# Optimization experiments

Measured on AMD Instinct MI355X. Metric: run time of the kernel, lower is better.

Reference implementation:

```python
import math
import jax, jax.numpy as jnp
import numpy as np

DIM = 1024
QK_DIM = 200
HIDDEN = 2 * DIM  # expansion_factor = 2
N = 8192


def setup_inputs() -> dict:
    key = jax.random.key(0)
    ks = jax.random.split(key, 8)
    s = 0.02
    return {
        "x": jax.random.normal(ks[0], (N, DIM), dtype=jnp.float32),
        "W_hidden": jax.random.normal(ks[1], (DIM, 2 * HIDDEN), dtype=jnp.float32) * s,
        "b_hidden": jnp.zeros((2 * HIDDEN,), dtype=jnp.float32),
        "W_qk": jax.random.normal(ks[2], (DIM, QK_DIM), dtype=jnp.float32) * s,
        "b_qk": jnp.zeros((QK_DIM,), dtype=jnp.float32),
        "gamma": 1.0 + jax.random.normal(ks[3], (2, QK_DIM), dtype=jnp.float32) * s,
        "beta": jnp.zeros((2, QK_DIM), dtype=jnp.float32),
        "W_out": jax.random.normal(ks[4], (HIDDEN, DIM), dtype=jnp.float32) * s,
        "b_out": jnp.zeros((DIM,), dtype=jnp.float32),
    }


def reference(x, W_hidden, b_hidden, W_qk, b_qk, gamma, beta, W_out, b_out):
    # to_hidden: Linear(dim -> 2*hidden) + SiLU, then chunk into v, gate
    hid = jax.nn.silu(x @ W_hidden + b_hidden)        # [N, 2H]
    v, gate = jnp.split(hid, 2, axis=-1)              # [N, H] each
    # to_qk: Linear(dim -> qk_dim) + SiLU
    qk = jax.nn.silu(x @ W_qk + b_qk)                 # [N, qk]
    # OffsetScale (heads=2): per-head affine on the shared qk
    q = qk * gamma[0] + beta[0]                       # [N, qk]
    k = qk * gamma[1] + beta[1]                       # [N, qk]
    # scores scaled by sqrt(dim) (module uses self.dim, not qk_dim)
    sim = (q @ k.T) * (1.0 / math.sqrt(x.shape[-1]))  # [N, N]
    # ReLU-squared attention (no softmax); dropout=0.0 -> identity
    attn = jnp.square(jax.nn.relu(sim))
    out = attn @ v                                    # [N, H]
    out = out * gate
    out = out @ W_out + b_out                         # [N, dim]
    # add_residual=True in this module multiplies by x
    return out * x
```

## Files before the change

kernel.cpp:

```cpp
#include <hip/hip_runtime.h>
#include <stdint.h>


typedef __bf16 bf16x8 __attribute__((ext_vector_type(8)));
typedef float f32x4 __attribute__((ext_vector_type(4)));

__device__ __forceinline__ uint16_t f2bf(float f) {
  uint32_t u = __builtin_bit_cast(uint32_t, f);
  u += 0x7fffu + ((u >> 16) & 1u);
  return (uint16_t)(u >> 16);
}
__device__ __forceinline__ float silu_f(float s) {
  return s / (1.f + __expf(-s));
}

__device__ __forceinline__ void gload16(const void* g, void* l) {
  __builtin_amdgcn_global_load_lds(
      (__attribute__((address_space(1))) void*)const_cast<void*>(g),
      (__attribute__((address_space(3))) void*)l, 16, 0, 0);
}


__global__ void cast_to_bf16(const float* __restrict__ in, uint16_t* __restrict__ out, int n4) {
  int i = blockIdx.x * blockDim.x + threadIdx.x;
  if (i < n4) {
    float4 f = ((const float4*)in)[i];
    ushort4 o;
    o.x = f2bf(f.x); o.y = f2bf(f.y); o.z = f2bf(f.z); o.w = f2bf(f.w);
    ((ushort4*)out)[i] = o;
  }
}

__global__ void transpose_cast_pad(const float* __restrict__ in, uint16_t* __restrict__ out,
                                   int R, int C, int Cp) {
  __shared__ float tile[32][33];
  int cb = blockIdx.x * 32;
  int rb = blockIdx.y * 32;
  int tx = threadIdx.x;
  int ty = threadIdx.y;
#pragma unroll
  for (int i = 0; i < 4; ++i) {
    int r = rb + ty + i * 8;
    int c = cb + tx;
    tile[ty + i * 8][tx] = (c < C) ? in[(size_t)r * C + c] : 0.f;
  }
  __syncthreads();
#pragma unroll
  for (int i = 0; i < 4; ++i) {
    int c = cb + ty + i * 8;
    if (c < Cp) out[(size_t)c * R + rb + tx] = f2bf(tile[tx][ty + i * 8]);
  }
}


struct EpiParams {
  const float* bias;
  const float* bias2;
  const float* g0;
  const float* b0;
  const float* g1;
  const float* b1;
  const uint16_t* gate;
  const float* x;
  uint16_t* o16a;
  uint16_t* o16b;
  uint16_t* oq;
  uint16_t* ok;
  float* o32;
};

__global__ __launch_bounds__(256) void k_hidqk(
    const uint16_t* __restrict__ A, const uint16_t* __restrict__ Bt, EpiParams p) {
  __shared__ __align__(16) uint16_t SH[128 * 64];
  uint16_t* As = SH;
  uint16_t* Bs = SH + 4096;

  const int tid = threadIdx.x;
  const int lane = tid & 63;
  const int wave = tid >> 6;
  const int wr = (wave >> 1) * 64;
  const int wc = (wave & 1) * 64;
  const int m0 = blockIdx.y * 128;
  const int n0 = blockIdx.x * 128;
  const int lda = 1024, ldb = 1024, K = 1024;

  f32x4 acc[4][4] = {};

  const int r0 = tid >> 2;
  const int q8 = (tid & 3) * 8;
  const uint16_t* gA0 = A + (size_t)(m0 + r0) * lda + q8;
  const uint16_t* gA1 = A + (size_t)(m0 + 64 + r0) * lda + q8;
  const uint16_t* gB0 = Bt + (size_t)(n0 + r0) * ldb + q8;
  const uint16_t* gB1 = Bt + (size_t)(n0 + 64 + r0) * ldb + q8;
  uint16_t* lA0 = As + wave * 512;
  uint16_t* lA1 = As + 2048 + wave * 512;
  uint16_t* lB0 = Bs + wave * 512;
  uint16_t* lB1 = Bs + 2048 + wave * 512;

  const int fr = lane & 15;
  const int rg = lane >> 4;
  const int kq = rg * 8;

  for (int k0 = 0; k0 < K; k0 += 32) {
    __syncthreads();
    gload16(gA0 + k0, lA0);
    gload16(gA1 + k0, lA1);
    gload16(gB0 + k0, lB0);
    gload16(gB1 + k0, lB1);
    __syncthreads();

    bf16x8 a[4], b[4];
#pragma unroll
    for (int i = 0; i < 4; ++i)
      a[i] = *(const bf16x8*)(As + (wr + i * 16 + fr) * 32 + kq);
#pragma unroll
    for (int j = 0; j < 4; ++j)
      b[j] = *(const bf16x8*)(Bs + (wc + j * 16 + fr) * 32 + kq);
#pragma unroll
    for (int i = 0; i < 4; ++i)
#pragma unroll
      for (int j = 0; j < 4; ++j)
        acc[i][j] = __builtin_amdgcn_mfma_f32_16x16x32_bf16(a[i], b[j], acc[i][j], 0, 0, 0);
  }

  if (n0 < 2048) {
    __syncthreads();
    uint16_t* ar = SH + wave * 2048;
    const int lrow = lane >> 3;
    const int mc = (lane & 7) * 8;
#pragma unroll
    for (int j = 0; j < 4; ++j) {
      const float bc = p.bias[n0 + wc + j * 16 + fr];
#pragma unroll
      for (int i = 0; i < 4; ++i)
#pragma unroll
        for (int r = 0; r < 4; ++r)
          ar[fr * 72 + i * 16 + rg * 4 + r] = f2bf(silu_f(acc[i][j][r] + bc));
#pragma unroll
      for (int rr = 0; rr < 2; ++rr) {
        bf16x8 v = *(const bf16x8*)(ar + (rr * 8 + lrow) * 72 + mc);
        *(bf16x8*)(p.o16a + (size_t)(n0 + wc + j * 16 + rr * 8 + lrow) * 8192 + m0 + wr + mc) = v;
      }
    }
  } else if (n0 < 4096) {
    __syncthreads();
    uint16_t* ar = SH + wave * 2048;
    const int lrow = lane >> 3;
    const int nc = (lane & 7) * 8;
    float bc[4];
#pragma unroll
    for (int j = 0; j < 4; ++j) bc[j] = p.bias[n0 + wc + j * 16 + fr];
#pragma unroll
    for (int i = 0; i < 4; ++i) {
#pragma unroll
      for (int j = 0; j < 4; ++j)
#pragma unroll
        for (int r = 0; r < 4; ++r)
          ar[(rg * 4 + r) * 72 + j * 16 + fr] = f2bf(silu_f(acc[i][j][r] + bc[j]));
#pragma unroll
      for (int rr = 0; rr < 2; ++rr) {
        bf16x8 v = *(const bf16x8*)(ar + (rr * 8 + lrow) * 72 + nc);
        *(bf16x8*)(p.o16b + (size_t)(m0 + wr + i * 16 + rr * 8 + lrow) * 2048 + (n0 - 2048) + wc + nc) = v;
      }
    }
  } else {
#pragma unroll
    for (int i = 0; i < 4; ++i) {
#pragma unroll
      for (int j = 0; j < 4; ++j) {
        const int row = m0 + wr + i * 16 + rg * 4;
        const int qc = n0 + wc + j * 16 + fr - 4096;
#pragma unroll
        for (int r = 0; r < 4; ++r) {
          float qv = 0.f, kv = 0.f;
          if (qc < 200) {
            float s = silu_f(acc[i][j][r] + p.bias2[qc]);
            qv = s * p.g0[qc] + p.b0[qc];
            kv = s * p.g1[qc] + p.b1[qc];
          }
          p.oq[(size_t)(row + r) * 256 + qc] = f2bf(qv);
          p.ok[(size_t)(row + r) * 256 + qc] = f2bf(kv);
        }
      }
    }
  }
}

__global__ __launch_bounds__(256) void k_attn(
    const uint16_t* __restrict__ Q,
    const uint16_t* __restrict__ Kt,
    uint16_t* __restrict__ attn) {
  __shared__ __align__(16) uint16_t As[128 * 128];
  __shared__ __align__(16) uint16_t Bs[128 * 128];

  const int tid = threadIdx.x;
  const int lane = tid & 63;
  const int wave = tid >> 6;
  const int wr = (wave >> 1) * 64;
  const int wc = (wave & 1) * 64;
  const int m0 = blockIdx.y * 128;
  const int n0 = blockIdx.x * 128;
  const int fr = lane & 15;
  const int rg = lane >> 4;

  f32x4 acc[4][4] = {};

  for (int ko = 0; ko < 256; ko += 128) {
    __syncthreads();
#pragma unroll
    for (int t = 0; t < 8; ++t) {
      const int s = t * 4 + wave;
      const int row = s * 4 + rg;
      const int log8 = fr ^ (row & 15);
      gload16(Q + (size_t)(m0 + row) * 256 + ko + log8 * 8, As + s * 512);
      gload16(Kt + (size_t)(n0 + row) * 256 + ko + log8 * 8, Bs + s * 512);
    }
    __syncthreads();

#pragma unroll
    for (int kc = 0; kc < 4; ++kc) {
      bf16x8 a[4], b[4];
#pragma unroll
      for (int i = 0; i < 4; ++i)
        a[i] = *(const bf16x8*)(As + (wr + i * 16 + fr) * 128 + (((kc * 4 + rg) ^ fr) * 8));
#pragma unroll
      for (int j = 0; j < 4; ++j)
        b[j] = *(const bf16x8*)(Bs + (wc + j * 16 + fr) * 128 + (((kc * 4 + rg) ^ fr) * 8));
#pragma unroll
      for (int i = 0; i < 4; ++i)
#pragma unroll
        for (int j = 0; j < 4; ++j)
          acc[i][j] = __builtin_amdgcn_mfma_f32_16x16x32_bf16(a[i], b[j], acc[i][j], 0, 0, 0);
    }
  }

  __syncthreads();
  uint16_t* sl0 = As + wave * 2304;
#pragma unroll
  for (int i = 0; i < 4; ++i) {
    uint16_t* sl = sl0 + (i & 1) * 1152;
#pragma unroll
    for (int j = 0; j < 4; ++j)
#pragma unroll
      for (int r = 0; r < 4; ++r) {
        float s = fmaxf(acc[i][j][r] * 0.03125f, 0.f);
        sl[(rg * 4 + r) * 72 + j * 16 + fr] = f2bf(s * s);
      }
    const int row = lane >> 2;
    const int c0 = (lane & 3) * 16;
    bf16x8 v0 = *(const bf16x8*)(sl + row * 72 + c0);
    bf16x8 v1 = *(const bf16x8*)(sl + row * 72 + c0 + 8);
    uint16_t* dst = attn + (size_t)(m0 + wr + i * 16 + row) * 8192 + (n0 + wc + c0);
    *(bf16x8*)(dst) = v0;
    *(bf16x8*)(dst + 8) = v1;
  }
}

__global__ __launch_bounds__(512) void k_pv(
    const uint16_t* __restrict__ A, int lda,
    const uint16_t* __restrict__ Bt, int ldb,
    int K, int nx, EpiParams p) {
  __shared__ __align__(16) uint16_t SH[(128 + 256) * 32];
  uint16_t* As = SH;
  uint16_t* Bs = SH + 4096;

  const int id = blockIdx.x;
  const int bx = (id >> 3) % nx;
  const int by = (id & 7) + 8 * (id / (8 * nx));
  const int m0 = by * 128;
  const int n0 = bx * 256;

  const int tid = threadIdx.x;
  const int lane = tid & 63;
  const int wave = tid >> 6;
  const int wr = (wave & 1) * 64;
  const int wc = (wave >> 1) * 64;

  f32x4 acc[4][4] = {};

  const int r0 = tid >> 2;
  const int q8 = (tid & 3) * 8;
  const uint16_t* gA  = A  + (size_t)(m0 + r0) * lda + q8;
  const uint16_t* gB0 = Bt + (size_t)(n0 + r0) * ldb + q8;
  const uint16_t* gB1 = Bt + (size_t)(n0 + 128 + r0) * ldb + q8;
  uint16_t* lA  = As + wave * 512;
  uint16_t* lB0 = Bs + wave * 512;
  uint16_t* lB1 = Bs + 4096 + wave * 512;

  const int fr = lane & 15;
  const int rg = lane >> 4;
  const int kq = rg * 8;

  for (int k0 = 0; k0 < K; k0 += 32) {
    __syncthreads();
    gload16(gA + k0, lA);
    gload16(gB0 + k0, lB0);
    gload16(gB1 + k0, lB1);
    __syncthreads();

    bf16x8 a[4], b[4];
#pragma unroll
    for (int i = 0; i < 4; ++i)
      a[i] = *(const bf16x8*)(As + (wr + i * 16 + fr) * 32 + kq);
#pragma unroll
    for (int j = 0; j < 4; ++j)
      b[j] = *(const bf16x8*)(Bs + (wc + j * 16 + fr) * 32 + kq);
#pragma unroll
    for (int i = 0; i < 4; ++i)
#pragma unroll
      for (int j = 0; j < 4; ++j)
        acc[i][j] = __builtin_amdgcn_mfma_f32_16x16x32_bf16(a[i], b[j], acc[i][j], 0, 0, 0);
  }

  __syncthreads();
  uint16_t* ar = SH + wave * 1536;
  const int lrow = lane >> 3;
  const int nc = (lane & 7) * 8;
#pragma unroll
  for (int i = 0; i < 4; ++i) {
#pragma unroll
    for (int j = 0; j < 4; ++j)
#pragma unroll
      for (int r = 0; r < 4; ++r)
        ar[(rg * 4 + r) * 72 + j * 16 + fr] = f2bf(acc[i][j][r]);
#pragma unroll
    for (int rr = 0; rr < 2; ++rr) {
      const size_t base = (size_t)(m0 + wr + i * 16 + rr * 8 + lrow) * 2048 + n0 + wc + nc;
      bf16x8 v = *(const bf16x8*)(ar + (rr * 8 + lrow) * 72 + nc);
      bf16x8 g = *(const bf16x8*)(p.gate + base);
      bf16x8 o;
#pragma unroll
      for (int e = 0; e < 8; ++e) o[e] = (__bf16)((float)v[e] * (float)g[e]);
      *(bf16x8*)(p.o16a + base) = o;
    }
  }
}

__global__ __launch_bounds__(256) void k_final(
    const uint16_t* __restrict__ A,
    const uint16_t* __restrict__ Bt, EpiParams p) {
  __shared__ __align__(16) uint16_t As[128 * 32];
  __shared__ __align__(16) uint16_t Bs[128 * 32];

  const int tid = threadIdx.x;
  const int lane = tid & 63;
  const int wave = tid >> 6;
  const int wr = (wave >> 1) * 64;
  const int wc = (wave & 1) * 64;
  const int m0 = blockIdx.y * 128;
  const int n0 = blockIdx.x * 128;
  const int lda = 2048, ldb = 2048, K = 2048;

  f32x4 acc[4][4] = {};

  const int r0 = tid >> 2;
  const int q8 = (tid & 3) * 8;
  const uint16_t* gA0 = A + (size_t)(m0 + r0) * lda + q8;
  const uint16_t* gA1 = A + (size_t)(m0 + 64 + r0) * lda + q8;
  const uint16_t* gB0 = Bt + (size_t)(n0 + r0) * ldb + q8;
  const uint16_t* gB1 = Bt + (size_t)(n0 + 64 + r0) * ldb + q8;
  uint16_t* lA0 = As + wave * 512;
  uint16_t* lA1 = As + 2048 + wave * 512;
  uint16_t* lB0 = Bs + wave * 512;
  uint16_t* lB1 = Bs + 2048 + wave * 512;

  const int fr = lane & 15;
  const int kq = (lane >> 4) * 8;

  for (int k0 = 0; k0 < K; k0 += 32) {
    __syncthreads();
    gload16(gA0 + k0, lA0);
    gload16(gA1 + k0, lA1);
    gload16(gB0 + k0, lB0);
    gload16(gB1 + k0, lB1);
    __syncthreads();

    bf16x8 a[4], b[4];
#pragma unroll
    for (int i = 0; i < 4; ++i)
      a[i] = *(const bf16x8*)(As + (wr + i * 16 + fr) * 32 + kq);
#pragma unroll
    for (int j = 0; j < 4; ++j)
      b[j] = *(const bf16x8*)(Bs + (wc + j * 16 + fr) * 32 + kq);
#pragma unroll
    for (int i = 0; i < 4; ++i)
#pragma unroll
      for (int j = 0; j < 4; ++j)
        acc[i][j] = __builtin_amdgcn_mfma_f32_16x16x32_bf16(a[i], b[j], acc[i][j], 0, 0, 0);
  }

#pragma unroll
  for (int i = 0; i < 4; ++i) {
#pragma unroll
    for (int j = 0; j < 4; ++j) {
      const int row = m0 + wr + i * 16 + (lane >> 4) * 4;
      const int col = n0 + wc + j * 16 + fr;
      const float bc = p.bias[col];
#pragma unroll
      for (int r = 0; r < 4; ++r) {
        size_t idx = (size_t)(row + r) * 1024 + col;
        p.o32[idx] = (acc[i][j][r] + bc) * p.x[idx];
      }
    }
  }
}


extern "C" void kernel_launch(void* const* d_in, const int* in_sizes, int n_in,
                              void* d_out, int out_size, void* d_ws, size_t ws_size,
                              hipStream_t stream) {
  const float* x        = (const float*)d_in[0];
  const float* W_hidden = (const float*)d_in[1];
  const float* b_hidden = (const float*)d_in[2];
  const float* W_qk     = (const float*)d_in[3];
  const float* b_qk     = (const float*)d_in[4];
  const float* gamma    = (const float*)d_in[5];
  const float* beta     = (const float*)d_in[6];
  const float* W_out    = (const float*)d_in[7];
  const float* b_out    = (const float*)d_in[8];
  float* out = (float*)d_out;

  const bool fullM = ws_size >= (236ull << 20);
  const size_t region0 = fullM ? (128ull << 20) : (64ull << 20);

  char* base = (char*)d_ws;
  uint16_t* xb    = (uint16_t*)(base);
  uint16_t* WhT   = (uint16_t*)(base + (16ull << 20));
  uint16_t* WqkT  = (uint16_t*)(base + (24ull << 20));
  uint16_t* attnB = (uint16_t*)(base);
  char* tail = base + region0;
  uint16_t* WoT   = (uint16_t*)(tail);
  uint16_t* q     = (uint16_t*)(tail + (4ull << 20));
  uint16_t* kk    = (uint16_t*)(tail + (8ull << 20));
  uint16_t* vT    = (uint16_t*)(tail + (12ull << 20));
  uint16_t* gate  = (uint16_t*)(tail + (44ull << 20));
  uint16_t* out2g = (uint16_t*)(tail + (76ull << 20));
  (void)in_sizes; (void)n_in; (void)out_size;

  cast_to_bf16<<<(8192 * 1024 / 4) / 256, 256, 0, stream>>>(x, xb, 8192 * 1024 / 4);
  transpose_cast_pad<<<dim3(4096 / 32, 1024 / 32), dim3(32, 8), 0, stream>>>(W_hidden, WhT, 1024, 4096, 4096);
  transpose_cast_pad<<<dim3(256 / 32, 1024 / 32), dim3(32, 8), 0, stream>>>(W_qk, WqkT, 1024, 200, 256);
  transpose_cast_pad<<<dim3(1024 / 32, 2048 / 32), dim3(32, 8), 0, stream>>>(W_out, WoT, 2048, 1024, 1024);

  {
    EpiParams p{};
    p.bias = b_hidden; p.bias2 = b_qk;
    p.g0 = gamma; p.b0 = beta; p.g1 = gamma + 200; p.b1 = beta + 200;
    p.o16a = vT; p.o16b = gate; p.oq = q; p.ok = kk;
    k_hidqk<<<dim3(34, 64), 256, 0, stream>>>(xb, WhT, p);
  }

  if (fullM) {
    k_attn<<<dim3(64, 64), 256, 0, stream>>>(q, kk, attnB);
    {
      EpiParams p{};
      p.gate = gate; p.o16a = out2g;
      k_pv<<<dim3(8 * 64), 512, 0, stream>>>(attnB, 8192, vT, 8192, 8192, 8, p);
    }
  } else {
    for (int s = 0; s < 2; ++s) {
      k_attn<<<dim3(64, 32), 256, 0, stream>>>(q + (size_t)s * 4096 * 256, kk, attnB);
      {
        EpiParams p{};
        p.gate = gate + (size_t)s * 4096 * 2048;
        p.o16a = out2g + (size_t)s * 4096 * 2048;
        k_pv<<<dim3(8 * 32), 512, 0, stream>>>(attnB, 8192, vT, 8192, 8192, 8, p);
      }
    }
  }

  {
    EpiParams p{};
    p.bias = b_out; p.x = x; p.o32 = out;
    k_final<<<dim3(8, 64), 256, 0, stream>>>(out2g, WoT, p);
  }
}
```

Measured before the change: 698.1 us.

## Shrink QK padding to 224 and use small 32-wide K tiles in attention score kernel

Q and K are now stored with a row stride of 224 instead of 256, which cuts the padded contraction length in the score GEMM from 256 to 224 and skips writing the unused padding columns. The attention kernel switches from two 128-wide K stages in 64KB of shared memory to seven 32-wide stages in small unswizzled buffers, with a separate epilogue buffer. This should raise occupancy and trim wasted MFMA work and global traffic, but it adds more barriers per tile and drops the XOR swizzle, so LDS bank conflicts may appear.

```diff
diff --git a/kernel.cpp b/kernel.cpp
--- a/kernel.cpp
+++ b/kernel.cpp
@@ -170,16 +170,18 @@
       for (int j = 0; j < 4; ++j) {
         const int row = m0 + wr + i * 16 + rg * 4;
         const int qc = n0 + wc + j * 16 + fr - 4096;
-#pragma unroll
-        for (int r = 0; r < 4; ++r) {
-          float qv = 0.f, kv = 0.f;
-          if (qc < 200) {
-            float s = silu_f(acc[i][j][r] + p.bias2[qc]);
-            qv = s * p.g0[qc] + p.b0[qc];
-            kv = s * p.g1[qc] + p.b1[qc];
+        if (qc < 224) {
+#pragma unroll
+          for (int r = 0; r < 4; ++r) {
+            float qv = 0.f, kv = 0.f;
+            if (qc < 200) {
+              float s = silu_f(acc[i][j][r] + p.bias2[qc]);
+              qv = s * p.g0[qc] + p.b0[qc];
+              kv = s * p.g1[qc] + p.b1[qc];
+            }
+            p.oq[(size_t)(row + r) * 224 + qc] = f2bf(qv);
+            p.ok[(size_t)(row + r) * 224 + qc] = f2bf(kv);
           }
-          p.oq[(size_t)(row + r) * 256 + qc] = f2bf(qv);
-          p.ok[(size_t)(row + r) * 256 + qc] = f2bf(kv);
         }
       }
     }
@@ -190,8 +192,9 @@
     const uint16_t* __restrict__ Q,
     const uint16_t* __restrict__ Kt,
     uint16_t* __restrict__ attn) {
-  __shared__ __align__(16) uint16_t As[128 * 128];
-  __shared__ __align__(16) uint16_t Bs[128 * 128];
+  __shared__ __align__(16) uint16_t As[128 * 32];
+  __shared__ __align__(16) uint16_t Bs[128 * 32];
+  __shared__ __align__(16) uint16_t Ep[4][2][16 * 72];
 
   const int tid = threadIdx.x;
   const int lane = tid & 63;
@@ -200,45 +203,50 @@
   const int wc = (wave & 1) * 64;
   const int m0 = blockIdx.y * 128;
   const int n0 = blockIdx.x * 128;
+  const int lda = 224, ldb = 224, K = 224;
+
+  f32x4 acc[4][4] = {};
+
+  const int r0 = tid >> 2;
+  const int q8 = (tid & 3) * 8;
+  const uint16_t* gA0 = Q + (size_t)(m0 + r0) * lda + q8;
+  const uint16_t* gA1 = Q + (size_t)(m0 + 64 + r0) * lda + q8;
+  const uint16_t* gB0 = Kt + (size_t)(n0 + r0) * ldb + q8;
+  const uint16_t* gB1 = Kt + (size_t)(n0 + 64 + r0) * ldb + q8;
+  uint16_t* lA0 = As + wave * 512;
+  uint16_t* lA1 = As + 2048 + wave * 512;
+  uint16_t* lB0 = Bs + wave * 512;
+  uint16_t* lB1 = Bs + 2048 + wave * 512;
+
   const int fr = lane & 15;
   const int rg = lane >> 4;
-
-  f32x4 acc[4][4] = {};
-
-  for (int ko = 0; ko < 256; ko += 128) {
-    __syncthreads();
-#pragma unroll
-    for (int t = 0; t < 8; ++t) {
-      const int s = t * 4 + wave;
-      const int row = s * 4 + rg;
-      const int log8 = fr ^ (row & 15);
-      gload16(Q + (size_t)(m0 + row) * 256 + ko + log8 * 8, As + s * 512);
-      gload16(Kt + (size_t)(n0 + row) * 256 + ko + log8 * 8, Bs + s * 512);
-    }
-    __syncthreads();
-
-#pragma unroll
-    for (int kc = 0; kc < 4; ++kc) {
-      bf16x8 a[4], b[4];
-#pragma unroll
-      for (int i = 0; i < 4; ++i)
-        a[i] = *(const bf16x8*)(As + (wr + i * 16 + fr) * 128 + (((kc * 4 + rg) ^ fr) * 8));
+  const int kq = rg * 8;
+
+  for (int k0 = 0; k0 < K; k0 += 32) {
+    __syncthreads();
+    gload16(gA0 + k0, lA0);
+    gload16(gA1 + k0, lA1);
+    gload16(gB0 + k0, lB0);
+    gload16(gB1 + k0, lB1);
+    __syncthreads();
+
+    bf16x8 a[4], b[4];
+#pragma unroll
+    for (int i = 0; i < 4; ++i)
+      a[i] = *(const bf16x8*)(As + (wr + i * 16 + fr) * 32 + kq);
+#pragma unroll
+    for (int j = 0; j < 4; ++j)
+      b[j] = *(const bf16x8*)(Bs + (wc + j * 16 + fr) * 32 + kq);
+#pragma unroll
+    for (int i = 0; i < 4; ++i)
 #pragma unroll
       for (int j = 0; j < 4; ++j)
-        b[j] = *(const bf16x8*)(Bs + (wc + j * 16 + fr) * 128 + (((kc * 4 + rg) ^ fr) * 8));
-#pragma unroll
-      for (int i = 0; i < 4; ++i)
-#pragma unroll
-        for (int j = 0; j < 4; ++j)
-          acc[i][j] = __builtin_amdgcn_mfma_f32_16x16x32_bf16(a[i], b[j], acc[i][j], 0, 0, 0);
-    }
-  }
-
-  __syncthreads();
-  uint16_t* sl0 = As + wave * 2304;
+        acc[i][j] = __builtin_amdgcn_mfma_f32_16x16x32_bf16(a[i], b[j], acc[i][j], 0, 0, 0);
+  }
+
 #pragma unroll
   for (int i = 0; i < 4; ++i) {
-    uint16_t* sl = sl0 + (i & 1) * 1152;
+    uint16_t* sl = Ep[wave][i & 1];
 #pragma unroll
     for (int j = 0; j < 4; ++j)
 #pragma unroll
@@ -459,7 +467,7 @@
     }
   } else {
     for (int s = 0; s < 2; ++s) {
-      k_attn<<<dim3(64, 32), 256, 0, stream>>>(q + (size_t)s * 4096 * 256, kk, attnB);
+      k_attn<<<dim3(64, 32), 256, 0, stream>>>(q + (size_t)s * 4096 * 224, kk, attnB);
       {
         EpiParams p{};
         p.gate = gate + (size_t)s * 4096 * 2048;
```

Measured after the change: 641.0 us. -8.2%, faster.
